# Optimization experiments

Hardware: AMD Instinct MI355X
Metric: run time of the kernel (lower is better)

The kernel has to match this reference:

```python
import jax, jax.numpy as jnp
import numpy as np

H = 40  # hidden size


def _gru_layer(x, wih, whh, bih, bhh):
    """PyTorch-convention GRU layer. x: [B,T,D], wih: [3H,D], whh: [3H,H]."""
    # Precompute input contributions for all timesteps at once.
    xp = jnp.einsum('btd,gd->btg', x, wih) + bih  # [B,T,3H]

    def step(h, xt):
        gh = h @ whh.T + bhh                      # [B,3H]
        xr, xz, xn = jnp.split(xt, 3, axis=-1)
        hr, hz, hn = jnp.split(gh, 3, axis=-1)
        r = jax.nn.sigmoid(xr + hr)
        z = jax.nn.sigmoid(xz + hz)
        n = jnp.tanh(xn + r * hn)
        h = (1.0 - z) * n + z * h
        return h, h

    h0 = jnp.zeros((x.shape[0], H), dtype=x.dtype)
    _, ys = jax.lax.scan(step, h0, xp.transpose(1, 0, 2))  # ys: [T,B,H]
    return ys.transpose(1, 0, 2)


def _mlp(h, w1, b1, w2, b2):
    a = jax.nn.leaky_relu(h @ w1.T + b1, negative_slope=0.01)
    return a @ w2.T + b2


def setup_inputs() -> dict:
    key = jax.random.key(0)
    ks = jax.random.split(key, 16)
    s = 1.0 / np.sqrt(H)
    u = lambda k, shape: jax.random.uniform(k, shape, jnp.float32, -s, s)
    x = jax.random.normal(ks[0], (2048, 512, 20), dtype=jnp.float32)
    inp = {
        'x': x,
        # lay1 layer-0 GRU (input dim 20)
        'g0_wih': u(ks[1], (3 * H, 20)),
        'g0_whh': u(ks[2], (3 * H, H)),
        'g0_bih': u(ks[3], (3 * H,)),
        'g0_bhh': u(ks[4], (3 * H,)),
        # 4 stacked GRUs with 40-dim input: lay1 layer-1, lay3, lay5, lay7
        'g_wih': u(ks[5], (4, 3 * H, H)),
        'g_whh': u(ks[6], (4, 3 * H, H)),
        'g_bih': u(ks[7], (4, 3 * H)),
        'g_bhh': u(ks[8], (4, 3 * H)),
        # MLP first linears (lay2, lay4, lay6, lay8 first Linear)
        'mlp_w1': u(ks[9], (4, H, H)),
        'mlp_b1': u(ks[10], (4, H)),
        # MLP second linears for lay2, lay4, lay6 (40->40)
        'mlp_w2': u(ks[11], (3, H, H)),
        'mlp_b2': u(ks[12], (3, H)),
        # lay8 final Linear(40,1)
        'w_last': u(ks[13], (1, H)),
        'b_last': u(ks[14], (1,)),
    }
    return inp


def reference(x, g0_wih, g0_whh, g0_bih, g0_bhh, g_wih, g_whh, g_bih, g_bhh,
              mlp_w1, mlp_b1, mlp_w2, mlp_b2, w_last, b_last):
    # lay1: 2-layer GRU
    h = _gru_layer(x, g0_wih, g0_whh, g0_bih, g0_bhh)
    h = _gru_layer(h, g_wih[0], g_whh[0], g_bih[0], g_bhh[0])
    # lay2..lay7: MLP then GRU, three times
    for i in range(3):
        h = _mlp(h, mlp_w1[i], mlp_b1[i], mlp_w2[i], mlp_b2[i])
        h = _gru_layer(h, g_wih[i + 1], g_whh[i + 1], g_bih[i + 1], g_bhh[i + 1])
    # lay8: Linear(40,40) + LeakyReLU + Linear(40,1)
    a = jax.nn.leaky_relu(h @ mlp_w1[3].T + mlp_b1[3], negative_slope=0.01)
    t = a @ w_last.T + b_last                     # [B,T,1]
    return jax.nn.sigmoid(t[:, -1])               # [B,1]
```

## Files before the change

kernel.cpp:

```cpp
#include <hip/hip_runtime.h>
#include <hip/hip_fp16.h>
#include <cstdint>
#include <cstddef>

#define T_STEPS 512
#define ROWSP   516
#define HID 40
#define GATES 120

typedef _Float16 half8 __attribute__((ext_vector_type(8)));
typedef _Float16 fp16x2 __attribute__((ext_vector_type(2)));
typedef float f32x4 __attribute__((ext_vector_type(4)));

__device__ __forceinline__ void wavesync() { asm volatile("s_waitcnt lgkmcnt(0)" ::: "memory"); }
__device__ __forceinline__ float bperm(int srclane, float v) {
    return __int_as_float(__builtin_amdgcn_ds_bpermute(srclane << 2, __float_as_int(v)));
}
__device__ __forceinline__ float sigm(float x) { return 1.f / (1.f + __expf(-x)); }

template<int J>
__device__ __forceinline__ fp16x2 ext2(half8 v) {
    return __builtin_shufflevector(v, v, 2 * J, 2 * J + 1);
}

#if __has_builtin(__builtin_amdgcn_fdot2)
__device__ __forceinline__ float fdot2(fp16x2 a, fp16x2 b, float c) {
    return __builtin_amdgcn_fdot2(a, b, c, false);
}
#else
__device__ __forceinline__ float fdot2(fp16x2 a, fp16x2 b, float c) {
    return c + (float)a[0] * (float)b[0] + (float)a[1] * (float)b[1];
}
#endif

__device__ __forceinline__ size_t rowoff(int row) {
    return ((size_t)(row >> 9) * ROWSP + (row & 511)) * GATES;
}

__global__ __launch_bounds__(256) void prep_pad(
    const float* __restrict__ w, const float* __restrict__ b,
    __half* __restrict__ out, int N, int K, int KPAD)
{
    const int idx = blockIdx.x * 256 + threadIdx.x;
    const int n = idx / KPAD, k = idx - n * KPAD;
    float v = 0.f;
    if (n < N) {
        if (k < K) v = w[n * K + k];
        else if (k == KPAD - 1) v = b[n];
    }
    out[idx] = __float2half(v);
}

__global__ __launch_bounds__(256) void prep_eff(
    const float* __restrict__ g_wih, const float* __restrict__ g_bih,
    const float* __restrict__ w2, const float* __restrict__ b2,
    __half* __restrict__ out)
{
    const int li  = blockIdx.y;
    const int idx = blockIdx.x * 256 + threadIdx.x;
    const int n = idx >> 6, k = idx & 63;
    float v = 0.f;
    if (n < GATES) {
        const float* wrow = g_wih + ((size_t)(li + 1) * GATES + n) * HID;
        if (k < HID) {
            for (int j = 0; j < HID; ++j) v += wrow[j] * w2[((size_t)li * HID + j) * HID + k];
        } else if (k == 63) {
            v = g_bih[(size_t)(li + 1) * GATES + n];
            for (int j = 0; j < HID; ++j) v += wrow[j] * b2[(size_t)li * HID + j];
        }
    }
    out[(size_t)li * 128 * 64 + idx] = __float2half(v);
}

__global__ __launch_bounds__(256) void prep_f16cvt(
    const float* __restrict__ w, _Float16* __restrict__ o, int n)
{
    const int i = blockIdx.x * 256 + threadIdx.x;
    if (i < n) o[i] = (_Float16)w[i];
}

template<int MODE>
__global__ __launch_bounds__(256) void precomp_mfma(
    const void* in_, _Float16* xp,
    const _Float16* __restrict__ wihpad,
    const _Float16* __restrict__ w1pad,
    int nrows)
{
    __shared__ _Float16 s_v[4][1024];
    const int tid  = threadIdx.x;
    const int wid  = tid >> 6, lane = tid & 63;
    const int g    = lane >> 4, r = lane & 15;

    constexpr int KP  = (MODE == 0) ? 32 : 64;
    constexpr int NKS = KP / 32;

    half8 bw[8][NKS];
    #pragma unroll
    for (int t = 0; t < 8; ++t)
        #pragma unroll
        for (int ks = 0; ks < NKS; ++ks)
            bw[t][ks] = *reinterpret_cast<const half8*>(wihpad + (t * 16 + r) * KP + ks * 32 + g * 8);

    half8 b1f[3][2];
    char* myv = nullptr;
    if constexpr (MODE == 2) {
        #pragma unroll
        for (int t = 0; t < 3; ++t)
            #pragma unroll
            for (int ks = 0; ks < 2; ++ks)
                b1f[t][ks] = *reinterpret_cast<const half8*>(w1pad + (t * 16 + r) * 64 + ks * 32 + g * 8);
        myv = (char*)&s_v[wid][0];
        uint4 z; z.x = z.y = z.z = z.w = 0u;
        *reinterpret_cast<uint4*>(myv + lane * 32)      = z;
        *reinterpret_cast<uint4*>(myv + lane * 32 + 16) = z;
        wavesync();
        if (lane < 16)
            *reinterpret_cast<_Float16*>(myv + lane * 128 + (126 ^ ((lane & 7) << 4))) = (_Float16)1.f;
        wavesync();
    }

    const int w0     = blockIdx.x * 4 + wid;
    const int stride = gridDim.x * 64;

    for (int rb = w0 * 16; rb < nrows; rb += stride) {
        half8 a0, a1;
        if constexpr (MODE == 0) {
            const float* xr = (const float*)in_ + (size_t)(rb + r) * 20;
            if (g < 2) {
                const float4 v0 = *reinterpret_cast<const float4*>(xr + g * 8);
                const float4 v1 = *reinterpret_cast<const float4*>(xr + g * 8 + 4);
                a0[0]=(_Float16)v0.x; a0[1]=(_Float16)v0.y; a0[2]=(_Float16)v0.z; a0[3]=(_Float16)v0.w;
                a0[4]=(_Float16)v1.x; a0[5]=(_Float16)v1.y; a0[6]=(_Float16)v1.z; a0[7]=(_Float16)v1.w;
            } else if (g == 2) {
                const float4 v0 = *reinterpret_cast<const float4*>(xr + 16);
                a0[0]=(_Float16)v0.x; a0[1]=(_Float16)v0.y; a0[2]=(_Float16)v0.z; a0[3]=(_Float16)v0.w;
                a0[4]=(_Float16)0.f; a0[5]=(_Float16)0.f; a0[6]=(_Float16)0.f; a0[7]=(_Float16)0.f;
            } else {
                #pragma unroll
                for (int j = 0; j < 8; ++j) a0[j] = (_Float16)0.f;
                a0[7] = (_Float16)1.f;
            }
        } else {
            const _Float16* hr = (const _Float16*)in_ + rowoff(rb + r);
            a0 = *reinterpret_cast<const half8*>(hr + g * 8);
            if (g == 0) {
                a1 = *reinterpret_cast<const half8*>(hr + 32);
            } else {
                #pragma unroll
                for (int j = 0; j < 8; ++j) a1[j] = (_Float16)0.f;
                if (g == 3) a1[7] = (_Float16)1.f;
            }
        }

        if constexpr (MODE == 2) {
            #pragma unroll
            for (int t = 0; t < 3; ++t) {
                f32x4 acc = {0.f, 0.f, 0.f, 0.f};
                acc = __builtin_amdgcn_mfma_f32_16x16x32_f16(a0, b1f[t][0], acc, 0, 0, 0);
                acc = __builtin_amdgcn_mfma_f32_16x16x32_f16(a1, b1f[t][1], acc, 0, 0, 0);
                const int n2 = (t * 16 + r) * 2;
                #pragma unroll
                for (int reg = 0; reg < 4; ++reg) {
                    const int m = g * 4 + reg;
                    float v = acc[reg];
                    v = v > 0.f ? v : 0.01f * v;
                    *reinterpret_cast<_Float16*>(myv + m * 128 + (n2 ^ ((m & 7) << 4))) = (_Float16)v;
                }
            }
            wavesync();
            const int sw = (r & 7) << 4;
            a0 = *reinterpret_cast<const half8*>(myv + r * 128 + ((g * 16) ^ sw));
            a1 = *reinterpret_cast<const half8*>(myv + r * 128 + ((64 + g * 16) ^ sw));
        }

        #pragma unroll
        for (int t = 0; t < 8; ++t) {
            f32x4 acc = {0.f, 0.f, 0.f, 0.f};
            acc = __builtin_amdgcn_mfma_f32_16x16x32_f16(a0, bw[t][0], acc, 0, 0, 0);
            if constexpr (NKS == 2)
                acc = __builtin_amdgcn_mfma_f32_16x16x32_f16(a1, bw[t][1], acc, 0, 0, 0);
            const int n = t * 16 + r;
            if (n < GATES) {
                #pragma unroll
                for (int reg = 0; reg < 4; ++reg) {
                    const int m = g * 4 + reg;
                    xp[rowoff(rb + m) + n] = (_Float16)acc[reg];
                }
            }
        }
    }
}

__global__ __launch_bounds__(64)
__attribute__((amdgpu_waves_per_eu(2, 2)))
void gru_recR(
    __half* __restrict__ xp,
    const _Float16* __restrict__ whh16,
    const float* __restrict__ bhh)
{
    __shared__ __align__(16) _Float16 s_w[GATES * HID];
    __shared__ __align__(16) _Float16 s_h[64];

    const int lane = threadIdx.x;
    const int e    = blockIdx.x;

    for (int idx = lane; idx < (GATES * HID) / 8; idx += 64)
        reinterpret_cast<uint4*>(s_w)[idx] = reinterpret_cast<const uint4*>(whh16)[idx];

    const int gA = lane;
    const int gB = (lane < 40) ? (80 + lane) : ((lane < 56) ? (24 + lane) : lane);
    const float bhA = bhh[gA], bhB = bhh[gB];

    __half* xpb = xp + (size_t)e * ROWSP * GATES;

    float hreg = 0.f;
    s_h[lane] = (_Float16)0.f;
    wavesync();

    fp16x2 wA[20], wB[20];
    {
        const _Float16* wrA = s_w + gA * HID;
        const _Float16* wrB = s_w + gB * HID;
        #pragma unroll
        for (int k = 0; k < 5; ++k) {
            const half8 wa = *reinterpret_cast<const half8*>(wrA + k * 8);
            const half8 wb = *reinterpret_cast<const half8*>(wrB + k * 8);
            wA[4*k+0] = ext2<0>(wa); wB[4*k+0] = ext2<0>(wb);
            wA[4*k+1] = ext2<1>(wa); wB[4*k+1] = ext2<1>(wb);
            wA[4*k+2] = ext2<2>(wa); wB[4*k+2] = ext2<2>(wb);
            wA[4*k+3] = ext2<3>(wa); wB[4*k+3] = ext2<3>(wb);
        }
    }
    wavesync();

    __half a0 = xpb[gA],             c0 = xpb[gB];
    __half a1 = xpb[GATES + gA],     c1 = xpb[GATES + gB];
    __half a2 = xpb[2 * GATES + gA], c2 = xpb[2 * GATES + gB];
    const __half* pfA = xpb + 3 * GATES + gA;
    const __half* pfB = xpb + 3 * GATES + gB;
    __half*       pst = xpb + lane;

    #pragma unroll 4
    for (int t = 0; t < T_STEPS; ++t) {
        const __half a3 = *pfA;  pfA += GATES;
        const __half c3 = *pfB;  pfB += GATES;

        const half8 p0 = *reinterpret_cast<const half8*>(&s_h[0]);
        const half8 p1 = *reinterpret_cast<const half8*>(&s_h[8]);
        const half8 p2 = *reinterpret_cast<const half8*>(&s_h[16]);
        const half8 p3 = *reinterpret_cast<const half8*>(&s_h[24]);
        const half8 p4 = *reinterpret_cast<const half8*>(&s_h[32]);

        float A0 = 0.f, A1 = 0.f, A2 = 0.f, A3 = 0.f;
        float B0 = 0.f, B1 = 0.f, B2 = 0.f, B3 = 0.f;
        A0 = fdot2(ext2<0>(p0), wA[ 0], A0); B0 = fdot2(ext2<0>(p0), wB[ 0], B0);
        A1 = fdot2(ext2<1>(p0), wA[ 1], A1); B1 = fdot2(ext2<1>(p0), wB[ 1], B1);
        A2 = fdot2(ext2<2>(p0), wA[ 2], A2); B2 = fdot2(ext2<2>(p0), wB[ 2], B2);
        A3 = fdot2(ext2<3>(p0), wA[ 3], A3); B3 = fdot2(ext2<3>(p0), wB[ 3], B3);
        A0 = fdot2(ext2<0>(p1), wA[ 4], A0); B0 = fdot2(ext2<0>(p1), wB[ 4], B0);
        A1 = fdot2(ext2<1>(p1), wA[ 5], A1); B1 = fdot2(ext2<1>(p1), wB[ 5], B1);
        A2 = fdot2(ext2<2>(p1), wA[ 6], A2); B2 = fdot2(ext2<2>(p1), wB[ 6], B2);
        A3 = fdot2(ext2<3>(p1), wA[ 7], A3); B3 = fdot2(ext2<3>(p1), wB[ 7], B3);
        A0 = fdot2(ext2<0>(p2), wA[ 8], A0); B0 = fdot2(ext2<0>(p2), wB[ 8], B0);
        A1 = fdot2(ext2<1>(p2), wA[ 9], A1); B1 = fdot2(ext2<1>(p2), wB[ 9], B1);
        A2 = fdot2(ext2<2>(p2), wA[10], A2); B2 = fdot2(ext2<2>(p2), wB[10], B2);
        A3 = fdot2(ext2<3>(p2), wA[11], A3); B3 = fdot2(ext2<3>(p2), wB[11], B3);
        A0 = fdot2(ext2<0>(p3), wA[12], A0); B0 = fdot2(ext2<0>(p3), wB[12], B0);
        A1 = fdot2(ext2<1>(p3), wA[13], A1); B1 = fdot2(ext2<1>(p3), wB[13], B1);
        A2 = fdot2(ext2<2>(p3), wA[14], A2); B2 = fdot2(ext2<2>(p3), wB[14], B2);
        A3 = fdot2(ext2<3>(p3), wA[15], A3); B3 = fdot2(ext2<3>(p3), wB[15], B3);
        A0 = fdot2(ext2<0>(p4), wA[16], A0); B0 = fdot2(ext2<0>(p4), wB[16], B0);
        A1 = fdot2(ext2<1>(p4), wA[17], A1); B1 = fdot2(ext2<1>(p4), wB[17], B1);
        A2 = fdot2(ext2<2>(p4), wA[18], A2); B2 = fdot2(ext2<2>(p4), wB[18], B2);
        A3 = fdot2(ext2<3>(p4), wA[19], A3); B3 = fdot2(ext2<3>(p4), wB[19], B3);

        const float shA = bhA + ((A0 + A2) + (A1 + A3));
        const float shB = bhB + ((B0 + B2) + (B1 + B3));
        const float xA  = __half2float(a0);
        const float xB  = __half2float(c0);
        const float sumA = xA + shA;
        const float sumB = xB + shB;
        const float zA = bperm(40 + lane, sumA);
        const float zB = bperm(16 + lane, sumB);

        if (lane < HID) {
            const float rr  = sigm(sumA);
            const float z   = sigm((lane < 24) ? zA : zB);
            const float pre = xB + rr * shB;
            const float ex  = __expf(-2.f * pre);
            const float nn  = (1.f - ex) / (1.f + ex);
            hreg = (1.f - z) * nn + z * hreg;
            s_h[lane] = (_Float16)hreg;
            *pst = __float2half(hreg);
        }
        pst += GATES;
        a0 = a1; c0 = c1; a1 = a2; c1 = c2; a2 = a3; c2 = c3;
        wavesync();
    }
}

__global__ __launch_bounds__(256) void final_head(
    const __half* __restrict__ xpbuf,
    float* __restrict__ outp,
    const float* __restrict__ w1, const float* __restrict__ b1,
    const float* __restrict__ wl, const float* __restrict__ bl, int n)
{
    __shared__ float s_w1[HID][HID + 1];
    __shared__ float s_b1[HID];
    __shared__ float s_wl[HID];
    for (int i = threadIdx.x; i < HID * HID; i += 256) s_w1[i / HID][i % HID] = w1[i];
    if (threadIdx.x < HID) { s_b1[threadIdx.x] = b1[threadIdx.x]; s_wl[threadIdx.x] = wl[threadIdx.x]; }
    __syncthreads();
    const int e = blockIdx.x * 256 + threadIdx.x;
    if (e >= n) return;

    const __half* hbase = xpbuf + ((size_t)e * ROWSP + (T_STEPS - 1)) * GATES;
    alignas(16) __half hx[HID];
    const uint4* hr = reinterpret_cast<const uint4*>(hbase);
    #pragma unroll
    for (int q = 0; q < HID / 8; ++q) reinterpret_cast<uint4*>(hx)[q] = hr[q];
    float h[HID];
    #pragma unroll
    for (int k = 0; k < HID; ++k) h[k] = __half2float(hx[k]);

    float acc = bl[0];
    #pragma unroll
    for (int u = 0; u < HID; ++u) {
        float a = s_b1[u];
        #pragma unroll
        for (int d = 0; d < HID; ++d) a += s_w1[u][d] * h[d];
        a = a > 0.f ? a : 0.01f * a;
        acc += a * s_wl[u];
    }
    outp[e] = 1.f / (1.f + __expf(-acc));
}

extern "C" void kernel_launch(void* const* d_in, const int* in_sizes, int n_in,
                              void* d_out, int out_size, void* d_ws, size_t ws_size,
                              hipStream_t stream)
{
    const float* x      = (const float*)d_in[0];
    const float* g0_wih = (const float*)d_in[1];
    const float* g0_whh = (const float*)d_in[2];
    const float* g0_bih = (const float*)d_in[3];
    const float* g0_bhh = (const float*)d_in[4];
    const float* g_wih  = (const float*)d_in[5];
    const float* g_whh  = (const float*)d_in[6];
    const float* g_bih  = (const float*)d_in[7];
    const float* g_bhh  = (const float*)d_in[8];
    const float* mlp_w1 = (const float*)d_in[9];
    const float* mlp_b1 = (const float*)d_in[10];
    const float* mlp_w2 = (const float*)d_in[11];
    const float* mlp_b2 = (const float*)d_in[12];
    const float* w_last = (const float*)d_in[13];
    const float* b_last = (const float*)d_in[14];

    const int B = in_sizes[0] / (T_STEPS * 20);
    float* out = (float*)d_out;

    __half* wsz    = (__half*)d_ws;
    __half* w1pad  = wsz;
    __half* effpad = wsz + 3 * 3072;
    __half* g0pad  = wsz + 9216 + 3 * 8192;
    __half* g1pad  = g0pad + 4096;
    _Float16* whh16 = (_Float16*)(wsz + 46080);
    _Float16* xpbuf = (_Float16*)(wsz + 70080);
    const size_t ws_rem = ws_size - 70080 * sizeof(__half);

    for (int li = 0; li < 3; ++li)
        prep_pad<<<dim3(12), dim3(256), 0, stream>>>(
            mlp_w1 + li * 1600, mlp_b1 + li * 40, w1pad + li * 3072, 40, 40, 64);
    prep_pad<<<dim3(16), dim3(256), 0, stream>>>(g0_wih, g0_bih, g0pad, 120, 20, 32);
    prep_pad<<<dim3(32), dim3(256), 0, stream>>>(g_wih, g_bih, g1pad, 120, 40, 64);
    prep_eff<<<dim3(32, 3), dim3(256), 0, stream>>>(g_wih, g_bih, mlp_w2, mlp_b2, effpad);
    prep_f16cvt<<<dim3(19), dim3(256), 0, stream>>>(g0_whh, whh16, 4800);
    prep_f16cvt<<<dim3(75), dim3(256), 0, stream>>>(g_whh, whh16 + 4800, 19200);

    const size_t per_e = (size_t)ROWSP * GATES * sizeof(__half);
    int CB = B;
    while ((size_t)CB * per_e > ws_rem && CB > 64) CB >>= 1;

    for (int c = 0; c < B; c += CB) {
        const int  nrows = CB * T_STEPS;
        const dim3 pgrd(nrows / 512), pblk(256);
        const dim3 rgrd(CB), rblk(64);
        const float* xc = x + (size_t)c * T_STEPS * 20;

        precomp_mfma<0><<<pgrd, pblk, 0, stream>>>(
            xc, xpbuf, (const _Float16*)g0pad, nullptr, nrows);
        gru_recR<<<rgrd, rblk, 0, stream>>>((__half*)xpbuf, whh16, g0_bhh);

        precomp_mfma<1><<<pgrd, pblk, 0, stream>>>(
            xpbuf, xpbuf, (const _Float16*)g1pad, nullptr, nrows);
        gru_recR<<<rgrd, rblk, 0, stream>>>((__half*)xpbuf, whh16 + 4800, g_bhh + 0 * 120);

        for (int li = 0; li < 3; ++li) {
            precomp_mfma<2><<<pgrd, pblk, 0, stream>>>(
                xpbuf, xpbuf, (const _Float16*)(effpad + li * 8192),
                (const _Float16*)(w1pad + li * 3072), nrows);
            gru_recR<<<rgrd, rblk, 0, stream>>>(
                (__half*)xpbuf, whh16 + 4800 + (li + 1) * 4800, g_bhh + (li + 1) * 120);
        }

        final_head<<<dim3((CB + 255) / 256), dim3(256), 0, stream>>>(
            (const __half*)xpbuf, out + c,
            mlp_w1 + 3 * 1600, mlp_b1 + 3 * 40, w_last, b_last, CB);
    }
}
```

Measured before the change: 1.671 ms.

## Broadcast hidden state via readlane and use fp32 FMAs in GRU recurrence

The recurrent GRU kernel now keeps weights in fp32 registers and replaces packed fp16 dot2 instructions with plain fp32 FMAs. The hidden state is broadcast to all lanes with 40 readlane instructions per step instead of a round trip through shared memory, which removes the LDS write/read latency from the serial dependency chain. The cost is twice as many multiply-add instructions, 40 scalar readlanes per step, and much higher register pressure (80 weight plus 40 hidden floats). The fp16 weight conversion kernels are dropped.

New measurement: 2.177 ms. 1.3x slower.

```diff
diff --git a/kernel.cpp b/kernel.cpp
--- a/kernel.cpp
+++ b/kernel.cpp
@@ -22,16 +22,6 @@
 __device__ __forceinline__ fp16x2 ext2(half8 v) {
     return __builtin_shufflevector(v, v, 2 * J, 2 * J + 1);
 }
-
-#if __has_builtin(__builtin_amdgcn_fdot2)
-__device__ __forceinline__ float fdot2(fp16x2 a, fp16x2 b, float c) {
-    return __builtin_amdgcn_fdot2(a, b, c, false);
-}
-#else
-__device__ __forceinline__ float fdot2(fp16x2 a, fp16x2 b, float c) {
-    return c + (float)a[0] * (float)b[0] + (float)a[1] * (float)b[1];
-}
-#endif
 
 __device__ __forceinline__ size_t rowoff(int row) {
     return ((size_t)(row >> 9) * ROWSP + (row & 511)) * GATES;
@@ -70,13 +60,6 @@
         }
     }
     out[(size_t)li * 128 * 64 + idx] = __float2half(v);
-}
-
-__global__ __launch_bounds__(256) void prep_f16cvt(
-    const float* __restrict__ w, _Float16* __restrict__ o, int n)
-{
-    const int i = blockIdx.x * 256 + threadIdx.x;
-    if (i < n) o[i] = (_Float16)w[i];
 }
 
 template<int MODE>
@@ -193,45 +176,38 @@
 
 __global__ __launch_bounds__(64)
 __attribute__((amdgpu_waves_per_eu(2, 2)))
-void gru_recR(
+void gru_recS(
     __half* __restrict__ xp,
-    const _Float16* __restrict__ whh16,
+    const float* __restrict__ whh,
     const float* __restrict__ bhh)
 {
-    __shared__ __align__(16) _Float16 s_w[GATES * HID];
-    __shared__ __align__(16) _Float16 s_h[64];
+    __shared__ __align__(16) float s_w[GATES * HID];
 
     const int lane = threadIdx.x;
     const int e    = blockIdx.x;
 
-    for (int idx = lane; idx < (GATES * HID) / 8; idx += 64)
-        reinterpret_cast<uint4*>(s_w)[idx] = reinterpret_cast<const uint4*>(whh16)[idx];
+    for (int idx = lane; idx < (GATES * HID) / 4; idx += 64)
+        reinterpret_cast<uint4*>(s_w)[idx] = reinterpret_cast<const uint4*>(whh)[idx];
 
     const int gA = lane;
     const int gB = (lane < 40) ? (80 + lane) : ((lane < 56) ? (24 + lane) : lane);
     const float bhA = bhh[gA], bhB = bhh[gB];
 
     __half* xpb = xp + (size_t)e * ROWSP * GATES;
+    wavesync();
+
+    float wA[40], wB[40];
+    #pragma unroll
+    for (int k = 0; k < 10; ++k) {
+        reinterpret_cast<float4*>(wA)[k] = *reinterpret_cast<const float4*>(s_w + gA * HID + 4 * k);
+        reinterpret_cast<float4*>(wB)[k] = *reinterpret_cast<const float4*>(s_w + gB * HID + 4 * k);
+    }
+    wavesync();
 
     float hreg = 0.f;
-    s_h[lane] = (_Float16)0.f;
-    wavesync();
-
-    fp16x2 wA[20], wB[20];
-    {
-        const _Float16* wrA = s_w + gA * HID;
-        const _Float16* wrB = s_w + gB * HID;
-        #pragma unroll
-        for (int k = 0; k < 5; ++k) {
-            const half8 wa = *reinterpret_cast<const half8*>(wrA + k * 8);
-            const half8 wb = *reinterpret_cast<const half8*>(wrB + k * 8);
-            wA[4*k+0] = ext2<0>(wa); wB[4*k+0] = ext2<0>(wb);
-            wA[4*k+1] = ext2<1>(wa); wB[4*k+1] = ext2<1>(wb);
-            wA[4*k+2] = ext2<2>(wa); wB[4*k+2] = ext2<2>(wb);
-            wA[4*k+3] = ext2<3>(wa); wB[4*k+3] = ext2<3>(wb);
-        }
-    }
-    wavesync();
+    float hb[40];
+    #pragma unroll
+    for (int j = 0; j < 40; ++j) hb[j] = 0.f;
 
     __half a0 = xpb[gA],             c0 = xpb[gB];
     __half a1 = xpb[GATES + gA],     c1 = xpb[GATES + gB];
@@ -240,40 +216,20 @@
     const __half* pfB = xpb + 3 * GATES + gB;
     __half*       pst = xpb + lane;
 
-    #pragma unroll 4
+    #pragma unroll 2
     for (int t = 0; t < T_STEPS; ++t) {
         const __half a3 = *pfA;  pfA += GATES;
         const __half c3 = *pfB;  pfB += GATES;
 
-        const half8 p0 = *reinterpret_cast<const half8*>(&s_h[0]);
-        const half8 p1 = *reinterpret_cast<const half8*>(&s_h[8]);
-        const half8 p2 = *reinterpret_cast<const half8*>(&s_h[16]);
-        const half8 p3 = *reinterpret_cast<const half8*>(&s_h[24]);
-        const half8 p4 = *reinterpret_cast<const half8*>(&s_h[32]);
-
         float A0 = 0.f, A1 = 0.f, A2 = 0.f, A3 = 0.f;
         float B0 = 0.f, B1 = 0.f, B2 = 0.f, B3 = 0.f;
-        A0 = fdot2(ext2<0>(p0), wA[ 0], A0); B0 = fdot2(ext2<0>(p0), wB[ 0], B0);
-        A1 = fdot2(ext2<1>(p0), wA[ 1], A1); B1 = fdot2(ext2<1>(p0), wB[ 1], B1);
-        A2 = fdot2(ext2<2>(p0), wA[ 2], A2); B2 = fdot2(ext2<2>(p0), wB[ 2], B2);
-        A3 = fdot2(ext2<3>(p0), wA[ 3], A3); B3 = fdot2(ext2<3>(p0), wB[ 3], B3);
-        A0 = fdot2(ext2<0>(p1), wA[ 4], A0); B0 = fdot2(ext2<0>(p1), wB[ 4], B0);
-        A1 = fdot2(ext2<1>(p1), wA[ 5], A1); B1 = fdot2(ext2<1>(p1), wB[ 5], B1);
-        A2 = fdot2(ext2<2>(p1), wA[ 6], A2); B2 = fdot2(ext2<2>(p1), wB[ 6], B2);
-        A3 = fdot2(ext2<3>(p1), wA[ 7], A3); B3 = fdot2(ext2<3>(p1), wB[ 7], B3);
-        A0 = fdot2(ext2<0>(p2), wA[ 8], A0); B0 = fdot2(ext2<0>(p2), wB[ 8], B0);
-        A1 = fdot2(ext2<1>(p2), wA[ 9], A1); B1 = fdot2(ext2<1>(p2), wB[ 9], B1);
-        A2 = fdot2(ext2<2>(p2), wA[10], A2); B2 = fdot2(ext2<2>(p2), wB[10], B2);
-        A3 = fdot2(ext2<3>(p2), wA[11], A3); B3 = fdot2(ext2<3>(p2), wB[11], B3);
-        A0 = fdot2(ext2<0>(p3), wA[12], A0); B0 = fdot2(ext2<0>(p3), wB[12], B0);
-        A1 = fdot2(ext2<1>(p3), wA[13], A1); B1 = fdot2(ext2<1>(p3), wB[13], B1);
-        A2 = fdot2(ext2<2>(p3), wA[14], A2); B2 = fdot2(ext2<2>(p3), wB[14], B2);
-        A3 = fdot2(ext2<3>(p3), wA[15], A3); B3 = fdot2(ext2<3>(p3), wB[15], B3);
-        A0 = fdot2(ext2<0>(p4), wA[16], A0); B0 = fdot2(ext2<0>(p4), wB[16], B0);
-        A1 = fdot2(ext2<1>(p4), wA[17], A1); B1 = fdot2(ext2<1>(p4), wB[17], B1);
-        A2 = fdot2(ext2<2>(p4), wA[18], A2); B2 = fdot2(ext2<2>(p4), wB[18], B2);
-        A3 = fdot2(ext2<3>(p4), wA[19], A3); B3 = fdot2(ext2<3>(p4), wB[19], B3);
-
+        #pragma unroll
+        for (int k = 0; k < 40; k += 4) {
+            A0 += hb[k+0] * wA[k+0];  B0 += hb[k+0] * wB[k+0];
+            A1 += hb[k+1] * wA[k+1];  B1 += hb[k+1] * wB[k+1];
+            A2 += hb[k+2] * wA[k+2];  B2 += hb[k+2] * wB[k+2];
+            A3 += hb[k+3] * wA[k+3];  B3 += hb[k+3] * wB[k+3];
+        }
         const float shA = bhA + ((A0 + A2) + (A1 + A3));
         const float shB = bhB + ((B0 + B2) + (B1 + B3));
         const float xA  = __half2float(a0);
@@ -283,17 +239,21 @@
         const float zA = bperm(40 + lane, sumA);
         const float zB = bperm(16 + lane, sumB);
 
-        if (lane < HID) {
-            const float rr  = sigm(sumA);
-            const float z   = sigm((lane < 24) ? zA : zB);
-            const float pre = xB + rr * shB;
-            const float ex  = __expf(-2.f * pre);
-            const float nn  = (1.f - ex) / (1.f + ex);
-            hreg = (1.f - z) * nn + z * hreg;
-            s_h[lane] = (_Float16)hreg;
-            *pst = __float2half(hreg);
-        }
+        const float rr  = sigm(sumA);
+        const float z   = sigm((lane < 24) ? zA : zB);
+        const float pre = xB + rr * shB;
+        const float ex  = __expf(-2.f * pre);
+        const float nn  = (1.f - ex) / (1.f + ex);
+        hreg = (1.f - z) * nn + z * hreg;
+
+        const int hi = __float_as_int(hreg);
+        #pragma unroll
+        for (int j = 0; j < 40; ++j)
+            hb[j] = __int_as_float(__builtin_amdgcn_readlane(hi, j));
+
+        if (lane < HID) *pst = __float2half(hreg);
         pst += GATES;
+
         a0 = a1; c0 = c1; a1 = a2; c1 = c2; a2 = a3; c2 = c3;
         wavesync();
     }
@@ -363,7 +323,6 @@
     __half* effpad = wsz + 3 * 3072;
     __half* g0pad  = wsz + 9216 + 3 * 8192;
     __half* g1pad  = g0pad + 4096;
-    _Float16* whh16 = (_Float16*)(wsz + 46080);
     _Float16* xpbuf = (_Float16*)(wsz + 70080);
     const size_t ws_rem = ws_size - 70080 * sizeof(__half);
 
@@ -373,8 +332,6 @@
     prep_pad<<<dim3(16), dim3(256), 0, stream>>>(g0_wih, g0_bih, g0pad, 120, 20, 32);
     prep_pad<<<dim3(32), dim3(256), 0, stream>>>(g_wih, g_bih, g1pad, 120, 40, 64);
     prep_eff<<<dim3(32, 3), dim3(256), 0, stream>>>(g_wih, g_bih, mlp_w2, mlp_b2, effpad);
-    prep_f16cvt<<<dim3(19), dim3(256), 0, stream>>>(g0_whh, whh16, 4800);
-    prep_f16cvt<<<dim3(75), dim3(256), 0, stream>>>(g_whh, whh16 + 4800, 19200);
 
     const size_t per_e = (size_t)ROWSP * GATES * sizeof(__half);
     int CB = B;
@@ -388,18 +345,18 @@
 
         precomp_mfma<0><<<pgrd, pblk, 0, stream>>>(
             xc, xpbuf, (const _Float16*)g0pad, nullptr, nrows);
-        gru_recR<<<rgrd, rblk, 0, stream>>>((__half*)xpbuf, whh16, g0_bhh);
+        gru_recS<<<rgrd, rblk, 0, stream>>>((__half*)xpbuf, g0_whh, g0_bhh);
 
         precomp_mfma<1><<<pgrd, pblk, 0, stream>>>(
             xpbuf, xpbuf, (const _Float16*)g1pad, nullptr, nrows);
-        gru_recR<<<rgrd, rblk, 0, stream>>>((__half*)xpbuf, whh16 + 4800, g_bhh + 0 * 120);
+        gru_recS<<<rgrd, rblk, 0, stream>>>((__half*)xpbuf, g_whh + 0 * 4800, g_bhh + 0 * 120);
 
         for (int li = 0; li < 3; ++li) {
             precomp_mfma<2><<<pgrd, pblk, 0, stream>>>(
                 xpbuf, xpbuf, (const _Float16*)(effpad + li * 8192),
                 (const _Float16*)(w1pad + li * 3072), nrows);
-            gru_recR<<<rgrd, rblk, 0, stream>>>(
-                (__half*)xpbuf, whh16 + 4800 + (li + 1) * 4800, g_bhh + (li + 1) * 120);
+            gru_recS<<<rgrd, rblk, 0, stream>>>(
+                (__half*)xpbuf, g_whh + (li + 1) * 4800, g_bhh + (li + 1) * 120);
         }
 
         final_head<<<dim3((CB + 255) / 256), dim3(256), 0, stream>>>(
```
